# Optimization experiments

Measured on AMD Instinct MI355X. Metric: run time of the kernel, lower is better.

Reference implementation:

```python
import jax, jax.numpy as jnp
import numpy as np

EMB = 512
HEADS = 8
HEAD_DIM = EMB // HEADS
GN_EPS = 1e-6
THETA_SCALE = 10000.0


def _multiply_by_i(x):
    # interleave: out[..., 2i] = -x[..., 2i+1], out[..., 2i+1] = x[..., 2i]
    return jnp.stack((-x[..., 1::2], x[..., ::2]), axis=-1).reshape(x.shape)


def _theta_shift(x, sin, cos):
    return x * cos + _multiply_by_i(x) * sin


def setup_inputs() -> dict:
    key = jax.random.key(0)
    ks = jax.random.split(key, 13)
    B, N, E = 2, 2048, EMB

    def xavier(k, out_dim, in_dim):
        std = (2.0 / (out_dim + in_dim)) ** 0.5
        return std * jax.random.normal(k, (out_dim, in_dim), dtype=jnp.float32)

    return {
        "query": jax.random.normal(ks[0], (B, N, E), dtype=jnp.float32),
        "k": jax.random.normal(ks[1], (B, N, E), dtype=jnp.float32),
        "v": jax.random.normal(ks[2], (B, N, E), dtype=jnp.float32),
        "Wq": xavier(ks[3], E, E), "bq": jnp.zeros((E,), jnp.float32),
        "Wk": xavier(ks[4], E, E), "bk": jnp.zeros((E,), jnp.float32),
        "Wv": xavier(ks[5], E, E), "bv": jnp.zeros((E,), jnp.float32),
        "Wg": xavier(ks[6], E, E), "bg": jnp.zeros((E,), jnp.float32),
        "Wo": xavier(ks[7], E, E), "bo": jnp.zeros((E,), jnp.float32),
    }


def reference(query, k, v, Wq, bq, Wk, bk, Wv, bv, Wg, bg, Wo, bo):
    B, N, E = query.shape
    H, D = HEADS, E // HEADS

    def proj(x, W, b):  # torch Linear: x @ W.T + b, then split heads -> [b h n d]
        return (x @ W.T + b).reshape(B, N, H, D).transpose(0, 2, 1, 3)

    q = proj(query, Wq, bq)
    kk = proj(k, Wk, bk)
    vv = proj(v, Wv, bv)

    # rotary-style theta shift; thetas repeated pairwise [t0,t0,t1,t1,...]
    thetas = jnp.repeat(1.0 / THETA_SCALE ** jnp.linspace(0.0, 1.0, D // 2), 2)
    angles = jnp.arange(N, dtype=jnp.float32)[:, None] * thetas[None, :]  # [n d]
    sin = jnp.sin(angles)[None, None]
    cos = jnp.cos(angles)[None, None]
    q = _theta_shift(q, sin, cos)
    kk = _theta_shift(kk, sin, cos)

    # decay-masked retention (softmax-free)
    gammas = 1.0 - jnp.exp(jnp.linspace(np.log(1 / 32), np.log(1 / 512), H)).astype(jnp.float32)
    pos = jnp.arange(N)
    dist = jnp.abs(pos[:, None] - pos[None, :]).astype(jnp.float32)
    causal = pos[:, None] >= pos[None, :]
    decay_mask = jnp.where(causal[None], gammas[:, None, None] ** dist[None], 0.0)  # [h n s]

    kk = kk / (D ** 0.5)
    sim = jnp.einsum('bhnd,bhsd->bhns', q, kk) * decay_mask[None]  # [b h n n]
    ret = jnp.einsum('bhns,bhsd->bhnd', sim, vv)

    # GroupNorm(groups=H, channels=H, affine=False) over (b n) samples -> per-(b,h,n) norm over d
    mean = ret.mean(axis=-1, keepdims=True)
    var = ret.var(axis=-1, keepdims=True)
    ret = (ret - mean) / jnp.sqrt(var + GN_EPS)

    ret = ret.transpose(0, 2, 1, 3).reshape(B, N, E)
    gate = jax.nn.silu(query @ Wg.T + bg)
    out = (ret * gate) @ Wo.T + bo
    return out
```

## Files before the change

kernel.cpp:

```cpp
#include <hip/hip_runtime.h>
#include <math.h>

typedef float f32x4 __attribute__((ext_vector_type(4)));
typedef short s16x8 __attribute__((ext_vector_type(8)));
typedef short s16x4 __attribute__((ext_vector_type(4)));

__device__ __forceinline__ short f2bf(float f) {
    unsigned u = __builtin_bit_cast(unsigned, f);
    unsigned r = u + 0x7FFFu + ((u >> 16) & 1u);
    return (short)(r >> 16);
}
__device__ __forceinline__ float bf2f(short h) {
    return __builtin_bit_cast(float, ((unsigned)(unsigned short)h) << 16);
}
__device__ __forceinline__ unsigned pack2(short a, short b) {
    return (unsigned)(unsigned short)a | ((unsigned)(unsigned short)b << 16);
}

__device__ __forceinline__ void split16v(const float* __restrict__ p,
                                         short* __restrict__ h,
                                         short* __restrict__ l) {
    f32x4 a0 = *(const f32x4*)(p);
    f32x4 a1 = *(const f32x4*)(p + 4);
    f32x4 a2 = *(const f32x4*)(p + 8);
    f32x4 a3 = *(const f32x4*)(p + 12);
    #pragma unroll
    for (int i = 0; i < 4; ++i) {
        short t0;
        t0 = f2bf(a0[i]); h[i]      = t0; l[i]      = f2bf(a0[i] - bf2f(t0));
        t0 = f2bf(a1[i]); h[4 + i]  = t0; l[4 + i]  = f2bf(a1[i] - bf2f(t0));
        t0 = f2bf(a2[i]); h[8 + i]  = t0; l[8 + i]  = f2bf(a2[i] - bf2f(t0));
        t0 = f2bf(a3[i]); h[12 + i] = t0; l[12 + i] = f2bf(a3[i] - bf2f(t0));
    }
}

__device__ __forceinline__ void gload16(const void* g, void* l) {
    __builtin_amdgcn_global_load_lds(
        (const __attribute__((address_space(1))) unsigned int*)g,
        (__attribute__((address_space(3))) unsigned int*)l,
        16, 0, 0);
}

__device__ __forceinline__ void decay_params(int h, int n0, float& l2g, int& stLo) {
    float lg0 = logf(1.0f / 32.0f), lg1 = logf(1.0f / 512.0f);
    float om = expf(lg0 + (float)h * (lg1 - lg0) * (1.0f / 7.0f));
    l2g = log2f(1.0f - om);
    int Dcut = (int)(11.5129255f / om) + 64;
    stLo = (n0 - Dcut) >> 6;
    if (stLo < 0) stLo = 0;
}

__global__ __launch_bounds__(256) void presplit_kernel(
    const float* __restrict__ W0, const float* __restrict__ W1,
    const float* __restrict__ W2, const float* __restrict__ W3,
    const float* __restrict__ W4,
    const float* __restrict__ X0, const float* __restrict__ X1,
    const float* __restrict__ X2,
    short* __restrict__ Wsp, short* __restrict__ Xsp,
    float2* __restrict__ SC)
{
    const int blk = blockIdx.x;
    const int t = threadIdx.x;
    short hbuf[16], lbuf[16];
    if (blk < 256) {
        const int w = blk >> 6, bi = blk & 63;
        const float* src = (w == 0) ? W0 : (w == 1) ? W1 : (w == 2) ? W2 : W3;
        const int idx = (bi * 256 + t) * 16;
        const int row = idx >> 9, k0 = idx & 511;
        const int ntile = row >> 7, r = row & 127;
        const int kstep = k0 >> 5, kk0 = k0 & 31;
        const int s = (r & 3) << 4;
        split16v(src + idx, hbuf, lbuf);
        short* hp = Wsp + (long)w * 524288 + (ntile * 16 + kstep) * 8192 + r * 32;
        short* lp = hp + 4096;
        const int oA = ((2 * kk0) ^ s) >> 1;
        const int oB = ((2 * kk0 + 16) ^ s) >> 1;
        *(s16x8*)(hp + oA) = *(s16x8*)(hbuf);
        *(s16x8*)(hp + oB) = *(s16x8*)(hbuf + 8);
        *(s16x8*)(lp + oA) = *(s16x8*)(lbuf);
        *(s16x8*)(lp + oB) = *(s16x8*)(lbuf + 8);
    } else if (blk < 320) {
        const int bi = blk - 256;
        const int idx = (bi * 256 + t) * 16;
        short* hi = Wsp + (long)4 * 524288;
        short* lo = hi + 262144;
        split16v(W4 + idx, hbuf, lbuf);
        *(s16x8*)(hi + idx)     = *(s16x8*)(hbuf);
        *(s16x8*)(hi + idx + 8) = *(s16x8*)(hbuf + 8);
        *(s16x8*)(lo + idx)     = *(s16x8*)(lbuf);
        *(s16x8*)(lo + idx + 8) = *(s16x8*)(lbuf + 8);
    } else if (blk < 1856) {
        const int b2 = blk - 320;
        const int x = b2 >> 9, bi = b2 & 511;
        const float* src = (x == 0) ? X0 : (x == 1) ? X1 : X2;
        const int idx = (bi * 256 + t) * 16;
        const int row = idx >> 9, k0 = idx & 511;
        const int mtile = row >> 6, r = row & 63;
        const int kstep = k0 >> 5, kk0 = k0 & 31;
        const int s = (r & 3) << 4;
        split16v(src + idx, hbuf, lbuf);
        short* hp = Xsp + (long)x * 4194304 + (mtile * 16 + kstep) * 4096 + r * 32;
        short* lp = hp + 2048;
        const int oA = ((2 * kk0) ^ s) >> 1;
        const int oB = ((2 * kk0 + 16) ^ s) >> 1;
        *(s16x8*)(hp + oA) = *(s16x8*)(hbuf);
        *(s16x8*)(hp + oB) = *(s16x8*)(hbuf + 8);
        *(s16x8*)(lp + oA) = *(s16x8*)(lbuf);
        *(s16x8*)(lp + oB) = *(s16x8*)(lbuf + 8);
    } else {
        const int gid = (blk - 1856) * 256 + t;
        const int pos = gid >> 5, pp = gid & 31;
        const float theta = powf(10000.0f, -(float)pp * (1.0f / 31.0f));
        const float ang = (float)pos * theta;
        SC[gid] = make_float2(cosf(ang), sinf(ang));
    }
}

__global__ __launch_bounds__(512, 4) void projqkvg_kernel(
    const short* __restrict__ Xsp, const short* __restrict__ Wsp,
    const float* __restrict__ bq, const float* __restrict__ bk,
    const float* __restrict__ bv, const float* __restrict__ bg,
    const float2* __restrict__ SC,
    short* __restrict__ Qh, short* __restrict__ Ql,
    short* __restrict__ Kh, short* __restrict__ Vth,
    float* __restrict__ G)
{
    __shared__ __align__(16) short SB[36864];

    const int fid = blockIdx.x + 4 * (blockIdx.y + 64 * blockIdx.z);
    const int mtile = fid & 63;
    const int rr = fid >> 6;
    const int mode = rr & 3;
    const int ntile = rr >> 2;
    const int m0 = mtile * 64, n0 = ntile * 128;

    const int xi = (mode == 1) ? 1 : (mode == 2) ? 2 : 0;
    const float* bias = (mode == 0) ? bq : (mode == 1) ? bk
                       : (mode == 2) ? bv : bg;

    const int t = threadIdx.x, lane = t & 63, wv = t >> 6;
    const int wm = wv >> 2, wn = wv & 3;
    const int quad = lane >> 4, l15 = lane & 15;

    const short* Xblk = Xsp + (long)xi * 4194304 + (long)mtile * 16 * 4096;
    const short* Wblk = Wsp + (long)mode * 524288 + (long)ntile * 16 * 8192;

    const int c0 = wv * 3;
    const short* gs[3];
    int gstp[3];
    #pragma unroll
    for (int i = 0; i < 3; ++i) {
        const int c = c0 + i;
        const bool isx = (c < 8);
        gs[i]   = isx ? (Xblk + c * 512 + lane * 8)
                      : (Wblk + (c - 8) * 512 + lane * 8);
        gstp[i] = isx ? 4096 : 8192;
    }

    auto STAGE = [&](int stg, int ks) {
        char* dstb = (char*)SB + stg * 24576 + c0 * 1024;
        #pragma unroll
        for (int i = 0; i < 3; ++i)
            gload16(gs[i] + ks * gstp[i], dstb + i * 1024);
    };

    const int sxw = (l15 & 3) << 4;
    int aoff[2], boff[2];
    #pragma unroll
    for (int s2 = 0; s2 < 2; ++s2)
        aoff[s2] = (wm * 32 + s2 * 16 + l15) * 64 + ((quad * 16) ^ sxw);
    #pragma unroll
    for (int s2 = 0; s2 < 2; ++s2)
        boff[s2] = 8192 + (wn * 32 + s2 * 16 + l15) * 64 + ((quad * 16) ^ sxw);

    f32x4 acc[2][2];
    #pragma unroll
    for (int i = 0; i < 2; ++i)
        #pragma unroll
        for (int j = 0; j < 2; ++j)
            acc[i][j] = (f32x4){0.f, 0.f, 0.f, 0.f};

    STAGE(0, 0);
    STAGE(1, 1);
    asm volatile("s_waitcnt vmcnt(3)" ::: "memory");
    __builtin_amdgcn_s_barrier();

    int cur = 0;
    for (int ks = 0; ks < 16; ++ks) {
        if (ks < 14) {
            int fill = cur + 2; if (fill >= 3) fill -= 3;
            STAGE(fill, ks + 2);
        }
        __builtin_amdgcn_sched_barrier(0);

        const char* stg = (const char*)SB + cur * 24576;
        s16x8 ah[2], al[2], bh[2], bl[2];
        #pragma unroll
        for (int s2 = 0; s2 < 2; ++s2) {
            ah[s2] = *(const s16x8*)(stg + aoff[s2]);
            al[s2] = *(const s16x8*)(stg + 4096 + aoff[s2]);
        }
        #pragma unroll
        for (int s2 = 0; s2 < 2; ++s2) {
            bh[s2] = *(const s16x8*)(stg + boff[s2]);
            bl[s2] = *(const s16x8*)(stg + 8192 + boff[s2]);
        }
        __builtin_amdgcn_s_setprio(1);
        #pragma unroll
        for (int i = 0; i < 2; ++i)
            #pragma unroll
            for (int j = 0; j < 2; ++j) {
                acc[i][j] = __builtin_amdgcn_mfma_f32_16x16x32_bf16(ah[i], bh[j], acc[i][j], 0, 0, 0);
                acc[i][j] = __builtin_amdgcn_mfma_f32_16x16x32_bf16(al[i], bh[j], acc[i][j], 0, 0, 0);
                acc[i][j] = __builtin_amdgcn_mfma_f32_16x16x32_bf16(ah[i], bl[j], acc[i][j], 0, 0, 0);
            }
        __builtin_amdgcn_s_setprio(0);

        if (ks < 14)       asm volatile("s_waitcnt vmcnt(3)" ::: "memory");
        else if (ks == 14) asm volatile("s_waitcnt vmcnt(0)" ::: "memory");
        __builtin_amdgcn_sched_barrier(0);
        __builtin_amdgcn_s_barrier();

        cur += 1; if (cur >= 3) cur -= 3;
    }

    __syncthreads();

    const int bb = m0 >> 11, posb = m0 & 2047;

    if (mode == 0) {
        short* Thi = SB + wv * 1280;
        short* Tlo = Thi + 640;
        const int head = (n0 >> 6) + (wn >> 1);
        const int dbase = (wn & 1) * 32;
        #pragma unroll
        for (int ms = 0; ms < 2; ++ms) {
            #pragma unroll
            for (int ns = 0; ns < 2; ++ns) {
                const int col = n0 + wn * 32 + ns * 16 + l15;
                const float bvv = bias[col];
                const int pp = (col & 63) >> 1;
                #pragma unroll
                for (int r = 0; r < 4; ++r) {
                    const int m = m0 + wm * 32 + ms * 16 + quad * 4 + r;
                    const int pos = m & 2047;
                    float x = acc[ms][ns][r] + bvv;
                    float prt = __shfl_xor(x, 1);
                    float2 sc = SC[pos * 32 + pp];
                    float y0 = x * sc.x - prt * sc.y;
                    float y1 = prt * sc.x + x * sc.y;
                    if (!(l15 & 1)) {
                        short h0 = f2bf(y0), h1 = f2bf(y1);
                        short l0 = f2bf(y0 - bf2f(h0)), l1 = f2bf(y1 - bf2f(h1));
                        const int o = (quad * 4 + r) * 40 + ns * 16 + l15;
                        *(unsigned*)&Thi[o] = pack2(h0, h1);
                        *(unsigned*)&Tlo[o] = pack2(l0, l1);
                    }
                }
            }
            const int mrow = wm * 32 + ms * 16;
            const int row = lane >> 2, ch = (lane & 3) * 8;
            s16x8 vh = *(const s16x8*)&Thi[row * 40 + ch];
            s16x8 vl = *(const s16x8*)&Tlo[row * 40 + ch];
            const long o = ((long)(bb * 8 + head) * 2048 + posb + mrow + row) * 64 + dbase + ch;
            *(s16x8*)(Qh + o) = vh;
            *(s16x8*)(Ql + o) = vl;
        }
    } else if (mode == 1) {
        short* Thi = SB + wv * 640;
        const int head = (n0 >> 6) + (wn >> 1);
        const int dbase = (wn & 1) * 32;
        #pragma unroll
        for (int ms = 0; ms < 2; ++ms) {
            #pragma unroll
            for (int ns = 0; ns < 2; ++ns) {
                const int col = n0 + wn * 32 + ns * 16 + l15;
                const float bvv = bias[col];
                const int pp = (col & 63) >> 1;
                #pragma unroll
                for (int r = 0; r < 4; ++r) {
                    const int m = m0 + wm * 32 + ms * 16 + quad * 4 + r;
                    const int pos = m & 2047;
                    float x = acc[ms][ns][r] + bvv;
                    float prt = __shfl_xor(x, 1);
                    float2 sc = SC[pos * 32 + pp];
                    float y0 = (x * sc.x - prt * sc.y) * 0.125f;
                    float y1 = (prt * sc.x + x * sc.y) * 0.125f;
                    if (!(l15 & 1)) {
                        const int o = (quad * 4 + r) * 40 + ns * 16 + l15;
                        *(unsigned*)&Thi[o] = pack2(f2bf(y0), f2bf(y1));
                    }
                }
            }
            const int mrow = wm * 32 + ms * 16;
            const int row = lane >> 2, ch = (lane & 3) * 8;
            s16x8 vh = *(const s16x8*)&Thi[row * 40 + ch];
            const long o = ((long)(bb * 8 + head) * 2048 + posb + mrow + row) * 64 + dbase + ch;
            *(s16x8*)(Kh + o) = vh;
        }
    } else if (mode == 2) {
        short* T2 = SB;
        #pragma unroll
        for (int ns = 0; ns < 2; ++ns) {
            const int col = n0 + wn * 32 + ns * 16 + l15;
            const float bvv = bias[col];
            #pragma unroll
            for (int ms = 0; ms < 2; ++ms) {
                s16x4 pk;
                #pragma unroll
                for (int r = 0; r < 4; ++r)
                    pk[r] = f2bf(acc[ms][ns][r] + bvv);
                *(s16x4*)&T2[(wn * 32 + ns * 16 + l15) * 72
                             + wm * 32 + ms * 16 + quad * 4] = pk;
            }
        }
        __syncthreads();
        #pragma unroll
        for (int pass = 0; pass < 2; ++pass) {
            const int row = pass * 64 + (t >> 3);
            const int ch = (t & 7) * 8;
            s16x8 v = *(const s16x8*)&T2[row * 72 + ch];
            const int head = (n0 >> 6) + (row >> 6);
            const int d = row & 63;
            const long o = ((long)(bb * 8 + head) * 64 + d) * 2048 + posb + ch;
            *(s16x8*)(Vth + o) = v;
        }
    } else {
        #pragma unroll
        for (int ns = 0; ns < 2; ++ns) {
            const int col = n0 + wn * 32 + ns * 16 + l15;
            const float bvv = bias[col];
            #pragma unroll
            for (int ms = 0; ms < 2; ++ms)
                #pragma unroll
                for (int r = 0; r < 4; ++r) {
                    const int m = m0 + wm * 32 + ms * 16 + quad * 4 + r;
                    float x = acc[ms][ns][r] + bvv;
                    G[(long)m * 512 + col] = x / (1.0f + expf(-x));
                }
        }
    }
}

__global__ __launch_bounds__(256) void attn_chunk_kernel(
    const short* __restrict__ Qh_g, const short* __restrict__ Ql_g,
    const short* __restrict__ Kh_g, const short* __restrict__ Vth_g,
    float* __restrict__ Racc)
{
    __shared__ __align__(16) short KhS[2][4608], VhS[2][4608];
    __shared__ __align__(16) short PhS[4352];

    const int fid = blockIdx.x;
    const int bh = fid & 15;
    const int rest = fid >> 4;
    const int qt = rest & 31;
    const int c  = rest >> 5;
    const int h = bh & 7;
    const int n0 = qt * 64;

    float l2g;
    int stLo;
    decay_params(h, n0, l2g, stLo);
    const int st0 = stLo + c * 16;
    if (st0 > qt) return;
    const int stHi = min(st0 + 15, qt);

    const int t = threadIdx.x, lane = t & 63, wv = t >> 6;
    const int quad = lane >> 4, l15 = lane & 15;
    const long base = (long)bh * 2048 * 64;

    float gneg[16];
    #pragma unroll
    for (int i = 0; i < 16; ++i)
        gneg[i] = exp2f(-(float)((i >> 2) * 16 + (i & 3)) * l2g);

    const int srow = t >> 2;
    const int scol = (t & 3) * 16;
    const int n = n0 + wv * 16 + l15;

    s16x8 qh[2], ql[2];
    {
        const short* qp  = Qh_g + base + (long)(n0 + wv * 16 + l15) * 64 + quad * 8;
        const short* qp2 = Ql_g + base + (long)(n0 + wv * 16 + l15) * 64 + quad * 8;
        qh[0] = *(const s16x8*)qp;
        qh[1] = *(const s16x8*)(qp + 32);
        ql[0] = *(const s16x8*)qp2;
        ql[1] = *(const s16x8*)(qp2 + 32);
    }

    f32x4 racc[4];
    #pragma unroll
    for (int i = 0; i < 4; ++i) racc[i] = (f32x4){0.f, 0.f, 0.f, 0.f};

    s16x8 pk0, pk1, pv0, pv1;
    {
        const long ko = base + (long)(st0 * 64 + srow) * 64 + scol;
        pk0 = *(const s16x8*)(Kh_g + ko);
        pk1 = *(const s16x8*)(Kh_g + ko + 8);
        const long vo = base + (long)srow * 2048 + st0 * 64 + scol;
        pv0 = *(const s16x8*)(Vth_g + vo);
        pv1 = *(const s16x8*)(Vth_g + vo + 8);
    }
    *(s16x8*)&KhS[0][srow * 72 + scol]     = pk0;
    *(s16x8*)&KhS[0][srow * 72 + scol + 8] = pk1;
    *(s16x8*)&VhS[0][srow * 72 + scol]     = pv0;
    *(s16x8*)&VhS[0][srow * 72 + scol + 8] = pv1;
    __syncthreads();

    int cur = 0;
    for (int st = st0; st <= stHi; ++st, cur ^= 1) {
        if (st < stHi) {
            const long ko = base + (long)((st + 1) * 64 + srow) * 64 + scol;
            pk0 = *(const s16x8*)(Kh_g + ko);
            pk1 = *(const s16x8*)(Kh_g + ko + 8);
            const long vo = base + (long)srow * 2048 + (st + 1) * 64 + scol;
            pv0 = *(const s16x8*)(Vth_g + vo);
            pv1 = *(const s16x8*)(Vth_g + vo + 8);
        }

        const short* khs = KhS[cur];
        const short* vhs = VhS[cur];
        const int s0 = st * 64;
        const float t0 = exp2f((float)(n - s0 - quad * 4) * l2g);

        #pragma unroll
        for (int sub = 0; sub < 4; ++sub) {
            const int ro = (sub * 16 + l15) * 72 + quad * 8;
            s16x8 kh0 = *(const s16x8*)&khs[ro];
            s16x8 kh1 = *(const s16x8*)&khs[ro + 32];
            f32x4 sacc = (f32x4){0.f, 0.f, 0.f, 0.f};
            sacc = __builtin_amdgcn_mfma_f32_16x16x32_bf16(kh0, qh[0], sacc, 0, 0, 0);
            sacc = __builtin_amdgcn_mfma_f32_16x16x32_bf16(kh1, qh[1], sacc, 0, 0, 0);
            sacc = __builtin_amdgcn_mfma_f32_16x16x32_bf16(kh0, ql[0], sacc, 0, 0, 0);
            sacc = __builtin_amdgcn_mfma_f32_16x16x32_bf16(kh1, ql[1], sacc, 0, 0, 0);

            const int sb = s0 + sub * 16 + quad * 4;
            s16x4 pkh;
            #pragma unroll
            for (int r = 0; r < 4; ++r) {
                const int s = sb + r;
                const float wgt = (n >= s) ? t0 * gneg[sub * 4 + r] : 0.0f;
                pkh[r] = f2bf(sacc[r] * wgt);
            }
            *(s16x4*)&PhS[(wv * 16 + l15) * 68 + sub * 16 + quad * 4] = pkh;
        }

        const int pro = (wv * 16 + l15) * 68 + quad * 8;
        s16x8 ph0 = *(const s16x8*)&PhS[pro];
        s16x8 ph1 = *(const s16x8*)&PhS[pro + 32];
        #pragma unroll
        for (int ds = 0; ds < 4; ++ds) {
            const int ro = (ds * 16 + l15) * 72 + quad * 8;
            s16x8 vh0 = *(const s16x8*)&vhs[ro];
            s16x8 vh1 = *(const s16x8*)&vhs[ro + 32];
            racc[ds] = __builtin_amdgcn_mfma_f32_16x16x32_bf16(ph0, vh0, racc[ds], 0, 0, 0);
            racc[ds] = __builtin_amdgcn_mfma_f32_16x16x32_bf16(ph1, vh1, racc[ds], 0, 0, 0);
        }

        if (st < stHi) {
            short* kd = KhS[cur ^ 1];
            short* vd = VhS[cur ^ 1];
            *(s16x8*)&kd[srow * 72 + scol]     = pk0;
            *(s16x8*)&kd[srow * 72 + scol + 8] = pk1;
            *(s16x8*)&vd[srow * 72 + scol]     = pv0;
            *(s16x8*)&vd[srow * 72 + scol + 8] = pv1;
        }
        __syncthreads();
    }

    float* dst = Racc + (long)((bh * 32 + qt) * 2 + c) * 4096;
    #pragma unroll
    for (int ds = 0; ds < 4; ++ds)
        #pragma unroll
        for (int r = 0; r < 4; ++r)
            dst[(wv * 16 + quad * 4 + r) * 64 + ds * 16 + l15] = racc[ds][r];
}

__global__ __launch_bounds__(256) void attn_finish_kernel(
    const float* __restrict__ Racc, const float* __restrict__ G,
    short* __restrict__ RGh)
{
    __shared__ __align__(16) short rgS[4608];

    const int fid = blockIdx.x;
    const int bh = fid & 15;
    const int qt = fid >> 4;
    const int h = bh & 7, b = bh >> 3;
    const int n0 = qt * 64;

    float l2g;
    int stLo;
    decay_params(h, n0, l2g, stLo);
    const int ntiles = qt - stLo + 1;
    const int nc = (ntiles + 15) >> 4;

    const int t = threadIdx.x, lane = t & 63, wv = t >> 6;
    const int quad = lane >> 4, l15 = lane & 15;

    const float* s0 = Racc + (long)((bh * 32 + qt) * 2) * 4096;
    f32x4 racc[4];
    #pragma unroll
    for (int ds = 0; ds < 4; ++ds)
        #pragma unroll
        for (int r = 0; r < 4; ++r) {
            const int o = (wv * 16 + quad * 4 + r) * 64 + ds * 16 + l15;
            float v = s0[o];
            if (nc > 1) v += s0[4096 + o];
            racc[ds][r] = v;
        }

    float mean[4], rstd[4];
    #pragma unroll
    for (int r = 0; r < 4; ++r) {
        float s = racc[0][r] + racc[1][r] + racc[2][r] + racc[3][r];
        s += __shfl_xor(s, 1); s += __shfl_xor(s, 2);
        s += __shfl_xor(s, 4); s += __shfl_xor(s, 8);
        mean[r] = s * (1.0f / 64.0f);
        float vs = 0.f;
        #pragma unroll
        for (int ds = 0; ds < 4; ++ds) {
            float d = racc[ds][r] - mean[r];
            vs += d * d;
        }
        vs += __shfl_xor(vs, 1); vs += __shfl_xor(vs, 2);
        vs += __shfl_xor(vs, 4); vs += __shfl_xor(vs, 8);
        rstd[r] = rsqrtf(vs * (1.0f / 64.0f) + 1e-6f);
    }

    short* rgH = rgS + wv * 1152;
    #pragma unroll
    for (int ds = 0; ds < 4; ++ds) {
        #pragma unroll
        for (int r = 0; r < 4; ++r) {
            const int nn = n0 + wv * 16 + quad * 4 + r;
            const int d = ds * 16 + l15;
            const long gi = ((long)(b * 2048 + nn)) * 512 + h * 64 + d;
            float rg = (racc[ds][r] - mean[r]) * rstd[r] * G[gi];
            float prt = __shfl_xor(rg, 1);
            if (!(l15 & 1)) {
                const int o = (quad * 4 + r) * 72 + ds * 16 + l15;
                *(unsigned*)&rgH[o] = pack2(f2bf(rg), f2bf(prt));
            }
        }
    }
    __syncthreads();
    #pragma unroll
    for (int p2 = 0; p2 < 2; ++p2) {
        const int row = p2 * 8 + (lane >> 3);
        const int ch = (lane & 7) * 8;
        s16x8 vh = *(const s16x8*)&rgH[row * 72 + ch];
        const int nn = n0 + wv * 16 + row;
        const long o = ((long)(b * 2048 + nn)) * 512 + h * 64 + ch;
        *(s16x8*)(RGh + o) = vh;
    }
}

__global__ __launch_bounds__(256) void projo_kernel(
    const short* __restrict__ RGh, const short* __restrict__ Woh_g,
    const float* __restrict__ bo, float* __restrict__ out)
{
    __shared__ __align__(16) char PB[46080];

    const short* Wol_g = Woh_g + 262144;
    const int t = threadIdx.x, lane = t & 63, wv = t >> 6;
    const int wm = wv >> 1, wn = wv & 1;
    const int quad = lane >> 4, l15 = lane & 15;
    const int m0 = blockIdx.y * 32, n0 = blockIdx.x * 128;

    f32x4 acc[4];
    #pragma unroll
    for (int j = 0; j < 4; ++j) acc[j] = (f32x4){0.f, 0.f, 0.f, 0.f};

    const int xrow = t >> 3, xcol = (t & 7) * 4;
    const int wrow = t >> 1, wcol = (t & 1) * 16;
    const long xbase = (long)(m0 + xrow) * 512 + xcol;
    const long wbase = (long)(n0 + wrow) * 512 + wcol;

    s16x4 px;
    s16x8 pw0, pw1, pw2, pw3;
    px  = *(const s16x4*)(RGh + xbase);
    pw0 = *(const s16x8*)(Woh_g + wbase);
    pw1 = *(const s16x8*)(Woh_g + wbase + 8);
    pw2 = *(const s16x8*)(Wol_g + wbase);
    pw3 = *(const s16x8*)(Wol_g + wbase + 8);

    {
        short* XhS = (short*)PB;
        short* WhS = XhS + 1280;
        short* WlS = XhS + 6400;
        *(s16x4*)&XhS[xrow * 40 + xcol]     = px;
        *(s16x8*)&WhS[wrow * 40 + wcol]     = pw0;
        *(s16x8*)&WhS[wrow * 40 + wcol + 8] = pw1;
        *(s16x8*)&WlS[wrow * 40 + wcol]     = pw2;
        *(s16x8*)&WlS[wrow * 40 + wcol + 8] = pw3;
    }
    __syncthreads();

    for (int k0 = 0; k0 < 512; k0 += 32) {
        const int cur = (k0 >> 5) & 1;
        const bool more = (k0 + 32 < 512);
        if (more) {
            const long xo = xbase + k0 + 32;
            const long wo = wbase + k0 + 32;
            px  = *(const s16x4*)(RGh + xo);
            pw0 = *(const s16x8*)(Woh_g + wo);
            pw1 = *(const s16x8*)(Woh_g + wo + 8);
            pw2 = *(const s16x8*)(Wol_g + wo);
            pw3 = *(const s16x8*)(Wol_g + wo + 8);
        }

        const short* XhS = (const short*)(PB + cur * 23040);
        const short* WhS = XhS + 1280;
        const short* WlS = XhS + 6400;
        s16x8 ah, bh[4], bl[4];
        {
            const int ro = (wm * 16 + l15) * 40 + quad * 8;
            ah = *(const s16x8*)&XhS[ro];
        }
        #pragma unroll
        for (int s = 0; s < 4; ++s) {
            const int ro = (wn * 64 + s * 16 + l15) * 40 + quad * 8;
            bh[s] = *(const s16x8*)&WhS[ro];
            bl[s] = *(const s16x8*)&WlS[ro];
        }
        #pragma unroll
        for (int j = 0; j < 4; ++j) {
            acc[j] = __builtin_amdgcn_mfma_f32_16x16x32_bf16(ah, bh[j], acc[j], 0, 0, 0);
            acc[j] = __builtin_amdgcn_mfma_f32_16x16x32_bf16(ah, bl[j], acc[j], 0, 0, 0);
        }

        if (more) {
            short* XhD = (short*)(PB + (cur ^ 1) * 23040);
            short* WhD = XhD + 1280;
            short* WlD = XhD + 6400;
            *(s16x4*)&XhD[xrow * 40 + xcol]     = px;
            *(s16x8*)&WhD[wrow * 40 + wcol]     = pw0;
            *(s16x8*)&WhD[wrow * 40 + wcol + 8] = pw1;
            *(s16x8*)&WlD[wrow * 40 + wcol]     = pw2;
            *(s16x8*)&WlD[wrow * 40 + wcol + 8] = pw3;
        }
        __syncthreads();
    }

    float* T = (float*)PB + wv * 1152;
    #pragma unroll
    for (int ns = 0; ns < 4; ++ns) {
        const int col = n0 + wn * 64 + ns * 16 + l15;
        const float bvv = bo[col];
        #pragma unroll
        for (int r = 0; r < 4; ++r)
            T[(quad * 4 + r) * 72 + ns * 16 + l15] = acc[ns][r] + bvv;
    }
    #pragma unroll
    for (int it = 0; it < 2; ++it) {
        const int row = it * 8 + (lane >> 3);
        const int ch = (lane & 7) * 8;
        f32x4 a = *(const f32x4*)&T[row * 72 + ch];
        f32x4 c = *(const f32x4*)&T[row * 72 + ch + 4];
        const long o = (long)(m0 + wm * 16 + row) * 512 + n0 + wn * 64 + ch;
        *(f32x4*)(out + o) = a;
        *(f32x4*)(out + o + 4) = c;
    }
}

extern "C" void kernel_launch(void* const* d_in, const int* in_sizes, int n_in,
                              void* d_out, int out_size, void* d_ws, size_t ws_size,
                              hipStream_t stream) {
    const float* query = (const float*)d_in[0];
    const float* kin   = (const float*)d_in[1];
    const float* vin   = (const float*)d_in[2];
    const float* Wq = (const float*)d_in[3];
    const float* bq = (const float*)d_in[4];
    const float* Wk = (const float*)d_in[5];
    const float* bk = (const float*)d_in[6];
    const float* Wv = (const float*)d_in[7];
    const float* bv = (const float*)d_in[8];
    const float* Wg = (const float*)d_in[9];
    const float* bg = (const float*)d_in[10];
    const float* Wo = (const float*)d_in[11];
    const float* bo = (const float*)d_in[12];

    short* S = (short*)d_ws;
    const long NE = 2097152;
    short* WSp = S;
    short* Xsp = S + 2621440;
    short* Qh  = Xsp + 12582912;
    short* Ql  = Qh + NE;
    short* Kh  = Ql + NE;
    short* Vth = Kh + NE;
    float* G   = (float*)(Vth + NE);
    short* RGh = (short*)(G + NE);
    float2* SC = (float2*)(RGh + NE);
    float* Racc = (float*)Xsp;

    presplit_kernel<<<2112, 256, 0, stream>>>(
        Wq, Wk, Wv, Wg, Wo, query, kin, vin, WSp, Xsp, SC);
    projqkvg_kernel<<<dim3(4, 64, 4), 512, 0, stream>>>(
        Xsp, WSp, bq, bk, bv, bg, SC, Qh, Ql, Kh, Vth, G);
    attn_chunk_kernel<<<1024, 256, 0, stream>>>(
        Qh, Ql, Kh, Vth, Racc);
    attn_finish_kernel<<<512, 256, 0, stream>>>(
        Racc, G, RGh);
    projo_kernel<<<dim3(4, 128), 256, 0, stream>>>(
        RGh, WSp + 4 * 524288, bo, (float*)d_out);
}
```

Measured before the change: 189.5 us.

## Fuse activation bf16 hi/lo split into projection GEMM, loading fp32 X directly

The presplit kernel no longer converts query/k/v into swizzled bf16 hi/lo tiles. Instead the QKV/gate projection kernel streams fp32 activation rows into LDS with an XOR swizzle and splits each value into bf16 hi and lo parts in registers before the MFMAs. This removes a full write and re-read of the split activation buffers (tens of MB) and shrinks the presplit launch. The cost is extra conversion ALU work inside the GEMM loop, which is repeated for each of the four output column tiles.

```diff
diff --git a/kernel.cpp b/kernel.cpp
--- a/kernel.cpp
+++ b/kernel.cpp
@@ -54,10 +54,7 @@
     const float* __restrict__ W0, const float* __restrict__ W1,
     const float* __restrict__ W2, const float* __restrict__ W3,
     const float* __restrict__ W4,
-    const float* __restrict__ X0, const float* __restrict__ X1,
-    const float* __restrict__ X2,
-    short* __restrict__ Wsp, short* __restrict__ Xsp,
-    float2* __restrict__ SC)
+    short* __restrict__ Wsp, float2* __restrict__ SC)
 {
     const int blk = blockIdx.x;
     const int t = threadIdx.x;
@@ -89,26 +86,8 @@
         *(s16x8*)(hi + idx + 8) = *(s16x8*)(hbuf + 8);
         *(s16x8*)(lo + idx)     = *(s16x8*)(lbuf);
         *(s16x8*)(lo + idx + 8) = *(s16x8*)(lbuf + 8);
-    } else if (blk < 1856) {
-        const int b2 = blk - 320;
-        const int x = b2 >> 9, bi = b2 & 511;
-        const float* src = (x == 0) ? X0 : (x == 1) ? X1 : X2;
-        const int idx = (bi * 256 + t) * 16;
-        const int row = idx >> 9, k0 = idx & 511;
-        const int mtile = row >> 6, r = row & 63;
-        const int kstep = k0 >> 5, kk0 = k0 & 31;
-        const int s = (r & 3) << 4;
-        split16v(src + idx, hbuf, lbuf);
-        short* hp = Xsp + (long)x * 4194304 + (mtile * 16 + kstep) * 4096 + r * 32;
-        short* lp = hp + 2048;
-        const int oA = ((2 * kk0) ^ s) >> 1;
-        const int oB = ((2 * kk0 + 16) ^ s) >> 1;
-        *(s16x8*)(hp + oA) = *(s16x8*)(hbuf);
-        *(s16x8*)(hp + oB) = *(s16x8*)(hbuf + 8);
-        *(s16x8*)(lp + oA) = *(s16x8*)(lbuf);
-        *(s16x8*)(lp + oB) = *(s16x8*)(lbuf + 8);
     } else {
-        const int gid = (blk - 1856) * 256 + t;
+        const int gid = (blk - 320) * 256 + t;
         const int pos = gid >> 5, pp = gid & 31;
         const float theta = powf(10000.0f, -(float)pp * (1.0f / 31.0f));
         const float ang = (float)pos * theta;
@@ -117,7 +96,8 @@
 }
 
 __global__ __launch_bounds__(512, 4) void projqkvg_kernel(
-    const short* __restrict__ Xsp, const short* __restrict__ Wsp,
+    const float* __restrict__ X0, const float* __restrict__ X1,
+    const float* __restrict__ X2, const short* __restrict__ Wsp,
     const float* __restrict__ bq, const float* __restrict__ bk,
     const float* __restrict__ bv, const float* __restrict__ bg,
     const float2* __restrict__ SC,
@@ -135,6 +115,7 @@
     const int m0 = mtile * 64, n0 = ntile * 128;
 
     const int xi = (mode == 1) ? 1 : (mode == 2) ? 2 : 0;
+    const float* Xf = (xi == 0) ? X0 : (xi == 1) ? X1 : X2;
     const float* bias = (mode == 0) ? bq : (mode == 1) ? bk
                        : (mode == 2) ? bv : bg;
 
@@ -142,19 +123,24 @@
     const int wm = wv >> 2, wn = wv & 3;
     const int quad = lane >> 4, l15 = lane & 15;
 
-    const short* Xblk = Xsp + (long)xi * 4194304 + (long)mtile * 16 * 4096;
     const short* Wblk = Wsp + (long)mode * 524288 + (long)ntile * 16 * 8192;
 
     const int c0 = wv * 3;
-    const short* gs[3];
+    const char* gs[3];
     int gstp[3];
     #pragma unroll
     for (int i = 0; i < 3; ++i) {
         const int c = c0 + i;
-        const bool isx = (c < 8);
-        gs[i]   = isx ? (Xblk + c * 512 + lane * 8)
-                      : (Wblk + (c - 8) * 512 + lane * 8);
-        gstp[i] = isx ? 4096 : 8192;
+        if (c < 8) {
+            const int u = c * 64 + lane;
+            const int row = u >> 3, ucol = u & 7;
+            gs[i] = (const char*)(Xf + (long)(m0 + row) * 512)
+                    + ((ucol ^ (row & 7)) << 4);
+            gstp[i] = 128;
+        } else {
+            gs[i] = (const char*)(Wblk + (c - 8) * 512 + lane * 8);
+            gstp[i] = 16384;
+        }
     }
 
     auto STAGE = [&](int stg, int ks) {
@@ -164,11 +150,14 @@
             gload16(gs[i] + ks * gstp[i], dstb + i * 1024);
     };
 
+    int aoff[2];
+    #pragma unroll
+    for (int s2 = 0; s2 < 2; ++s2) {
+        const int row = wm * 32 + s2 * 16 + l15;
+        aoff[s2] = row * 128 + ((quad * 32) ^ ((row & 7) << 4));
+    }
     const int sxw = (l15 & 3) << 4;
-    int aoff[2], boff[2];
-    #pragma unroll
-    for (int s2 = 0; s2 < 2; ++s2)
-        aoff[s2] = (wm * 32 + s2 * 16 + l15) * 64 + ((quad * 16) ^ sxw);
+    int boff[2];
     #pragma unroll
     for (int s2 = 0; s2 < 2; ++s2)
         boff[s2] = 8192 + (wn * 32 + s2 * 16 + l15) * 64 + ((quad * 16) ^ sxw);
@@ -197,8 +186,16 @@
         s16x8 ah[2], al[2], bh[2], bl[2];
         #pragma unroll
         for (int s2 = 0; s2 < 2; ++s2) {
-            ah[s2] = *(const s16x8*)(stg + aoff[s2]);
-            al[s2] = *(const s16x8*)(stg + 4096 + aoff[s2]);
+            f32x4 x0 = *(const f32x4*)(stg + aoff[s2]);
+            f32x4 x1 = *(const f32x4*)(stg + (aoff[s2] ^ 16));
+            s16x8 hv, lv;
+            #pragma unroll
+            for (int j = 0; j < 4; ++j) {
+                short hh;
+                hh = f2bf(x0[j]); hv[j]     = hh; lv[j]     = f2bf(x0[j] - bf2f(hh));
+                hh = f2bf(x1[j]); hv[4 + j] = hh; lv[4 + j] = f2bf(x1[j] - bf2f(hh));
+            }
+            ah[s2] = hv; al[s2] = lv;
         }
         #pragma unroll
         for (int s2 = 0; s2 < 2; ++s2) {
@@ -693,10 +690,10 @@
     float2* SC = (float2*)(RGh + NE);
     float* Racc = (float*)Xsp;
 
-    presplit_kernel<<<2112, 256, 0, stream>>>(
-        Wq, Wk, Wv, Wg, Wo, query, kin, vin, WSp, Xsp, SC);
+    presplit_kernel<<<576, 256, 0, stream>>>(
+        Wq, Wk, Wv, Wg, Wo, WSp, SC);
     projqkvg_kernel<<<dim3(4, 64, 4), 512, 0, stream>>>(
-        Xsp, WSp, bq, bk, bv, bg, SC, Qh, Ql, Kh, Vth, G);
+        query, kin, vin, WSp, bq, bk, bv, bg, SC, Qh, Ql, Kh, Vth, G);
     attn_chunk_kernel<<<1024, 256, 0, stream>>>(
         Qh, Ql, Kh, Vth, Racc);
     attn_finish_kernel<<<512, 256, 0, stream>>>(
```

New measurement: 198.5 us. +4.8%, slower.
